# Optimization experiments

Hardware: AMD Instinct MI355X
Metric: run time of the kernel (lower is better)

Reference implementation:

```python
import math
import jax, jax.numpy as jnp
import numpy as np

HEAD_SIZE = 64
DEPTH = 0

def lambda_init_fn(depth):
    depth = depth + 1
    return 0.8 - 0.6 * math.exp(-0.3 * depth)

def setup_inputs() -> dict:
    key = jax.random.key(0)
    ks = jax.random.split(key, 9)
    B, T, C = 4, 4096, 1024
    H2 = 2 * HEAD_SIZE  # 128
    return {
        "x":  jax.random.normal(ks[0], (B, T, C), dtype=jnp.float32),
        "Wq": jax.random.normal(ks[1], (C, H2), dtype=jnp.float32) * (C ** -0.5),
        "Wk": jax.random.normal(ks[2], (C, H2), dtype=jnp.float32) * (C ** -0.5),
        "Wv": jax.random.normal(ks[3], (C, H2), dtype=jnp.float32) * (C ** -0.5),
        "lambda_q1": jax.random.normal(ks[4], (HEAD_SIZE,), dtype=jnp.float32) * 0.1,
        "lambda_q2": jax.random.normal(ks[5], (HEAD_SIZE,), dtype=jnp.float32) * 0.1,
        "lambda_k1": jax.random.normal(ks[6], (HEAD_SIZE,), dtype=jnp.float32) * 0.1,
        "lambda_k2": jax.random.normal(ks[7], (HEAD_SIZE,), dtype=jnp.float32) * 0.1,
    }

def reference(x, Wq, Wk, Wv, lambda_q1, lambda_q2, lambda_k1, lambda_k2):
    B, T, C = x.shape
    q = x @ Wq  # (B,T,2*hs)
    k = x @ Wk
    v = x @ Wv  # (B,T,2*hs)
    q1, q2 = jnp.split(q, 2, axis=-1)
    k1, k2 = jnp.split(k, 2, axis=-1)
    scale = 1.0 / math.sqrt(HEAD_SIZE)
    w1 = jnp.einsum('btd,bsd->bts', q1, k1) * scale  # (B,T,T)
    w2 = jnp.einsum('btd,bsd->bts', q2, k2) * scale
    causal = jnp.tril(jnp.ones((T, T), dtype=bool))
    neg_inf = jnp.float32(-jnp.inf)
    w1 = jnp.where(causal, w1, neg_inf)
    w2 = jnp.where(causal, w2, neg_inf)
    lam1 = jnp.exp(jnp.sum(lambda_q1 * lambda_k1))
    lam2 = jnp.exp(jnp.sum(lambda_q2 * lambda_k2))
    lam = lam1 - lam2 + lambda_init_fn(DEPTH)
    weights = jax.nn.softmax(w1, axis=-1) - lam * jax.nn.softmax(w2, axis=-1)
    out = jnp.einsum('bts,bsd->btd', weights, v)  # (B,T,2*hs)
    return out
```

## Files before the change

kernel.cpp:

```cpp
#include <hip/hip_runtime.h>
#include <hip/hip_bf16.h>

typedef __bf16 bf16x8 __attribute__((ext_vector_type(8)));
typedef float f32x4 __attribute__((ext_vector_type(4)));

#define LAMBDA_INIT 0.3555090675909693f
#define CEXP 0.18033688011112042f

#define K_OFF   ((size_t)16384 * 128)
#define VT_OFF  ((size_t)2 * 16384 * 128)
#define PART_OFF_BYTES ((size_t)12582912)
#define REC_FLOATS 4160

__device__ __forceinline__ unsigned short f2bf(float f) {
    __hip_bfloat16 h = __float2bfloat16(f);
    unsigned short u;
    __builtin_memcpy(&u, &h, 2);
    return u;
}
__device__ __forceinline__ float bf2f(unsigned short u) {
    unsigned int x = ((unsigned int)u) << 16;
    float f;
    __builtin_memcpy(&f, &x, 4);
    return f;
}
__device__ __forceinline__ unsigned int cvt_pk_bf16(float a, float b) {
    unsigned int r;
    asm volatile("v_cvt_pk_bf16_f32 %0, %1, %2" : "=v"(r) : "v"(a), "v"(b));
    return r;
}

__global__ __launch_bounds__(256) void prep_wt(
    const float* __restrict__ Wq, const float* __restrict__ Wk,
    const float* __restrict__ Wv, unsigned short* __restrict__ WT) {
    const int kt = blockIdx.x, nt = blockIdx.y, mat = blockIdx.z;
    const float* W = (mat == 0) ? Wq : (mat == 1) ? Wk : Wv;
    unsigned short* O = WT + (size_t)mat * 128 * 1024;
    __shared__ float tb[64][65];
    const int r = threadIdx.x >> 2, c4 = (threadIdx.x & 3) * 16;
    for (int j = 0; j < 4; ++j) {
        float4 v = *(const float4*)&W[(size_t)(kt * 64 + r) * 128 + nt * 64 + c4 + j * 4];
        tb[r][c4 + j * 4 + 0] = v.x;
        tb[r][c4 + j * 4 + 1] = v.y;
        tb[r][c4 + j * 4 + 2] = v.z;
        tb[r][c4 + j * 4 + 3] = v.w;
    }
    __syncthreads();
    unsigned short tmp[16];
    for (int j = 0; j < 16; ++j) tmp[j] = f2bf(tb[c4 + j][r]);
    *(uint4*)&O[(size_t)(nt * 64 + r) * 1024 + kt * 64 + c4] = *(uint4*)&tmp[0];
    *(uint4*)&O[(size_t)(nt * 64 + r) * 1024 + kt * 64 + c4 + 8] = *(uint4*)&tmp[8];
}

__global__ __launch_bounds__(256, 3) void qkv_gemm(
    const float* __restrict__ x, const unsigned short* __restrict__ WT,
    unsigned short* __restrict__ qkv) {
    const int tid = threadIdx.x;
    const int l = tid & 63, w = tid >> 6;
    const int g = l >> 4, i16 = l & 15;
    const int row0 = blockIdx.x * 64;
    const int mat = blockIdx.y;
    const unsigned short* Wt = WT + (size_t)mat * 128 * 1024;

    __shared__ unsigned short xs[64][72];
    __shared__ unsigned short wt[128][72];

    f32x4 acc[8];
    const f32x4 z4 = {0.f, 0.f, 0.f, 0.f};
    for (int nb = 0; nb < 8; ++nb) acc[nb] = z4;

    const int xr = tid >> 4;
    const int xc = (tid & 15) * 4;
    const int wn = tid >> 3;
    const int wk8 = (tid & 7) * 8;
    const float* xp0 = &x[(size_t)(row0 + xr) * 1024 + xc];
    const unsigned short* wp0 = &Wt[(size_t)wn * 1024 + wk8];

    float4 ax0, ax1, ax2, ax3, bx0, bx1, bx2, bx3;
    uint4 aw0, aw1, aw2, aw3, bw0, bw1, bw2, bw3;

#define QI(k0_, X0, X1, X2, X3, W0, W1, W2, W3) do {                        \
        X0 = *(const float4*)&xp0[(k0_)];                                   \
        X1 = *(const float4*)&xp0[16 * 1024 + (k0_)];                       \
        X2 = *(const float4*)&xp0[32 * 1024 + (k0_)];                       \
        X3 = *(const float4*)&xp0[48 * 1024 + (k0_)];                       \
        W0 = *(const uint4*)&wp0[(k0_)];                                    \
        W1 = *(const uint4*)&wp0[32 * 1024 + (k0_)];                        \
        W2 = *(const uint4*)&wp0[64 * 1024 + (k0_)];                        \
        W3 = *(const uint4*)&wp0[96 * 1024 + (k0_)];                        \
    } while (0)

#define QS(X0, X1, X2, X3, W0, W1, W2, W3) do {                             \
        *(ushort4*)&xs[xr +  0][xc] = make_ushort4(f2bf(X0.x), f2bf(X0.y), f2bf(X0.z), f2bf(X0.w)); \
        *(ushort4*)&xs[xr + 16][xc] = make_ushort4(f2bf(X1.x), f2bf(X1.y), f2bf(X1.z), f2bf(X1.w)); \
        *(ushort4*)&xs[xr + 32][xc] = make_ushort4(f2bf(X2.x), f2bf(X2.y), f2bf(X2.z), f2bf(X2.w)); \
        *(ushort4*)&xs[xr + 48][xc] = make_ushort4(f2bf(X3.x), f2bf(X3.y), f2bf(X3.z), f2bf(X3.w)); \
        *(uint4*)&wt[wn +  0][wk8] = W0;                                    \
        *(uint4*)&wt[wn + 32][wk8] = W1;                                    \
        *(uint4*)&wt[wn + 64][wk8] = W2;                                    \
        *(uint4*)&wt[wn + 96][wk8] = W3;                                    \
    } while (0)

#define QMFMA() do {                                                        \
        bf16x8 af0 = *(const bf16x8*)&xs[w * 16 + i16][8 * g];              \
        bf16x8 af1 = *(const bf16x8*)&xs[w * 16 + i16][32 + 8 * g];         \
        _Pragma("unroll")                                                   \
        for (int nb = 0; nb < 8; ++nb) {                                    \
            bf16x8 b0 = *(const bf16x8*)&wt[nb * 16 + i16][8 * g];          \
            bf16x8 b1 = *(const bf16x8*)&wt[nb * 16 + i16][32 + 8 * g];     \
            acc[nb] = __builtin_amdgcn_mfma_f32_16x16x32_bf16(af0, b0, acc[nb], 0, 0, 0); \
            acc[nb] = __builtin_amdgcn_mfma_f32_16x16x32_bf16(af1, b1, acc[nb], 0, 0, 0); \
        }                                                                   \
    } while (0)

    QI(0, ax0, ax1, ax2, ax3, aw0, aw1, aw2, aw3);
    QI(64, bx0, bx1, bx2, bx3, bw0, bw1, bw2, bw3);
    #pragma unroll 1
    for (int k0 = 0; k0 < 1024; k0 += 128) {
        __syncthreads();
        QS(ax0, ax1, ax2, ax3, aw0, aw1, aw2, aw3);
        if (k0 + 128 < 1024) QI(k0 + 128, ax0, ax1, ax2, ax3, aw0, aw1, aw2, aw3);
        __syncthreads();
        QMFMA();
        __syncthreads();
        QS(bx0, bx1, bx2, bx3, bw0, bw1, bw2, bw3);
        if (k0 + 192 < 1024) QI(k0 + 192, bx0, bx1, bx2, bx3, bw0, bw1, bw2, bw3);
        __syncthreads();
        QMFMA();
    }
#undef QI
#undef QS
#undef QMFMA

    __syncthreads();
    unsigned short(*ts)[136] = (unsigned short(*)[136]) & wt[0][0];
    const float qscale = (mat == 0) ? CEXP : 1.0f;
    for (int nb = 0; nb < 8; ++nb)
        for (int r = 0; r < 4; ++r)
            ts[w * 16 + g * 4 + r][nb * 16 + i16] = f2bf(acc[nb][r] * qscale);
    __syncthreads();

    const int bq = row0 >> 12;
    const int s = (row0 >> 6) & 63;
    if (mat == 0) {
        unsigned short* outp = qkv + (size_t)row0 * 128;
        #pragma unroll
        for (int it = 0; it < 4; ++it) {
            int tr = it * 16 + (tid >> 4), dv0 = (tid & 15) * 8;
            *(uint4*)&outp[tr * 128 + dv0] = *(const uint4*)&ts[tr][dv0];
        }
    } else if (mat == 1) {
        unsigned short* kimg = qkv + K_OFF + ((size_t)(bq * 64 + s) * 2) * 4096;
        #pragma unroll
        for (int it = 0; it < 4; ++it) {
            int lin = it * 256 + tid;
            int branch_ = (lin >> 9) & 1;
            int region = (lin >> 6) & 7;
            int slot = lin & 63;
            int row = (region >> 1) * 16 + (slot & 15);
            int d = branch_ * 64 + (region & 1) * 32 + (slot >> 4) * 8;
            uint4 vv = *(const uint4*)&ts[row][d];
            *(uint4*)&kimg[(size_t)branch_ * 4096 + (region * 64 + slot) * 8] = vv;
        }
    } else {
        unsigned short* vimg = qkv + VT_OFF + (size_t)(bq * 64 + s) * 8192;
        #pragma unroll
        for (int it = 0; it < 4; ++it) {
            int lin = it * 256 + tid;
            int region = lin >> 6;
            int slot = lin & 63;
            int dv = (region >> 1) * 16 + (slot & 15);
            int kv0 = (region & 1) * 32 + (slot >> 4) * 8;
            unsigned short tmp[8];
            #pragma unroll
            for (int e = 0; e < 8; ++e) tmp[e] = ts[kv0 + e][dv];
            *(uint4*)&vimg[(region * 64 + slot) * 8] = *(uint4*)tmp;
        }
    }
}

__global__ __launch_bounds__(256, 3) void diff_attn_pair(
    const unsigned short* __restrict__ q, const unsigned short* __restrict__ kimg,
    const unsigned short* __restrict__ vimg,
    float* __restrict__ part, int ncs) {
    const int bx = blockIdx.x, b = blockIdx.y;
    const int c = blockIdx.z >> 1, branch = blockIdx.z & 1;
    const int bxe = (c & 1) ? (31 - bx) : bx;
    const int t_o = 63 - 2 * bxe, t_e = t_o - 1;
    const int n = t_o + 1;
    const int s_lo = (c * n) >> ncs, smax = ((c + 1) * n) >> ncs;

    if (s_lo >= smax) return;

    const int tid = threadIdx.x;
    const int l = tid & 63, w = tid >> 6;
    const int gq = l >> 4, i16 = l & 15;
    const float NEGINF = -__builtin_inff();

    __shared__ unsigned short ksf[2][4096];
    __shared__ unsigned short psf[8192];

    float* recA = part + ((((size_t)(b * 64 + t_e) << ncs) + c) * 2 + branch) * REC_FLOATS;
    float* recB = part + ((((size_t)(b * 64 + t_o) << ncs) + c) * 2 + branch) * REC_FLOATS;
    const bool emptyA = (s_lo > t_e);

    const size_t bbase = (size_t)b * 4096;
    const unsigned short* kimg_b = kimg + (size_t)b * 524288;
    const unsigned short* vimg_b = vimg + (size_t)b * 524288;
    const int tid8 = tid * 8;
    const int l8 = l * 8;
    const f32x4 z4 = {0.f, 0.f, 0.f, 0.f};

    bf16x8 qfA[2], qfB[2];
    #pragma unroll
    for (int cc = 0; cc < 2; ++cc) {
        qfA[cc] = *(const bf16x8*)&q[(bbase + t_e * 64 + w * 16 + i16) * 128 + branch * 64 + cc * 32 + 8 * gq];
        qfB[cc] = *(const bf16x8*)&q[(bbase + t_o * 64 + w * 16 + i16) * 128 + branch * 64 + cc * 32 + 8 * gq];
    }

    float lsumA = 0.f, lsumB = 0.f;
    f32x4 acc[2][4][2];
    for (int qs = 0; qs < 2; ++qs)
        for (int qg = 0; qg < 4; ++qg)
            for (int j = 0; j < 2; ++j) acc[qs][qg][j] = z4;

    int pdst[4];
    #pragma unroll
    for (int cb = 0; cb < 4; ++cb)
        pdst[cb] = ((w * 2 + (cb >> 1)) * 64 + ((cb & 1) * 2 + (gq >> 1)) * 16 + i16) * 8 + (gq & 1) * 4;

    uint4 kr0, kr1;
    bf16x8 vb00, vb01, vb10, vb11;

#define K_ISSUE(s_) do {                                                            \
        const unsigned short* kp = &kimg_b[((size_t)(s_) * 2 + branch) * 4096];     \
        kr0 = *(const uint4*)&kp[tid8];                                             \
        kr1 = *(const uint4*)&kp[tid8 + 2048];                                      \
    } while (0)
#define V_ISSUE(s_) do {                                                            \
        const unsigned short* vp = &vimg_b[(size_t)(s_) * 8192 + w * 2048];         \
        vb00 = *(const bf16x8*)&vp[l8];                                             \
        vb01 = *(const bf16x8*)&vp[512 + l8];                                       \
        vb10 = *(const bf16x8*)&vp[1024 + l8];                                      \
        vb11 = *(const bf16x8*)&vp[1536 + l8];                                      \
    } while (0)

    K_ISSUE(s_lo);
    V_ISSUE(s_lo);
    int pb = 0;
    #pragma unroll 1
    for (int s = s_lo; s < smax; ++s) {
        *(uint4*)&ksf[pb][tid8] = kr0;
        *(uint4*)&ksf[pb][tid8 + 2048] = kr1;
        if (s + 1 < smax) K_ISSUE(s + 1);
        __syncthreads();
        const bool aAct = (s != t_o);

        f32x4 scA[4], scB[4];
        for (int cb = 0; cb < 4; ++cb) { scA[cb] = z4; scB[cb] = z4; }
        __builtin_amdgcn_s_setprio(1);
        #pragma unroll
        for (int cb = 0; cb < 4; ++cb)
            for (int cc = 0; cc < 2; ++cc) {
                bf16x8 kf = *(const bf16x8*)&ksf[pb][((cb * 2 + cc) * 64 + l) * 8];
                scA[cb] = __builtin_amdgcn_mfma_f32_16x16x32_bf16(kf, qfA[cc], scA[cb], 0, 0, 0);
                scB[cb] = __builtin_amdgcn_mfma_f32_16x16x32_bf16(kf, qfB[cc], scB[cb], 0, 0, 0);
            }
        __builtin_amdgcn_s_setprio(0);

        if (aAct) {
            if (s == t_e) {
                int ql = w * 16 + i16;
                for (int cb = 0; cb < 4; ++cb)
                    for (int r = 0; r < 4; ++r)
                        if (cb * 16 + gq * 4 + r > ql) scA[cb][r] = NEGINF;
            }
            #pragma unroll
            for (int cb = 0; cb < 4; ++cb) {
                float p0 = exp2f(scA[cb][0]);
                float p1 = exp2f(scA[cb][1]);
                float p2 = exp2f(scA[cb][2]);
                float p3 = exp2f(scA[cb][3]);
                lsumA += (p0 + p1) + (p2 + p3);
                uint2 pw;
                pw.x = cvt_pk_bf16(p0, p1);
                pw.y = cvt_pk_bf16(p2, p3);
                *(uint2*)&psf[pdst[cb]] = pw;
            }
        }
        {
            if (s == t_o) {
                int ql = w * 16 + i16;
                for (int cb = 0; cb < 4; ++cb)
                    for (int r = 0; r < 4; ++r)
                        if (cb * 16 + gq * 4 + r > ql) scB[cb][r] = NEGINF;
            }
            #pragma unroll
            for (int cb = 0; cb < 4; ++cb) {
                float p0 = exp2f(scB[cb][0]);
                float p1 = exp2f(scB[cb][1]);
                float p2 = exp2f(scB[cb][2]);
                float p3 = exp2f(scB[cb][3]);
                lsumB += (p0 + p1) + (p2 + p3);
                uint2 pw;
                pw.x = cvt_pk_bf16(p0, p1);
                pw.y = cvt_pk_bf16(p2, p3);
                *(uint2*)&psf[4096 + pdst[cb]] = pw;
            }
        }
        __syncthreads();

        __builtin_amdgcn_s_setprio(1);
        if (aAct) {
            #pragma unroll
            for (int qg = 0; qg < 4; ++qg) {
                bf16x8 pa0 = *(const bf16x8*)&psf[(qg * 2 + 0) * 512 + l8];
                bf16x8 pa1 = *(const bf16x8*)&psf[(qg * 2 + 1) * 512 + l8];
                acc[0][qg][0] = __builtin_amdgcn_mfma_f32_16x16x32_bf16(pa0, vb00, acc[0][qg][0], 0, 0, 0);
                acc[0][qg][0] = __builtin_amdgcn_mfma_f32_16x16x32_bf16(pa1, vb01, acc[0][qg][0], 0, 0, 0);
                acc[0][qg][1] = __builtin_amdgcn_mfma_f32_16x16x32_bf16(pa0, vb10, acc[0][qg][1], 0, 0, 0);
                acc[0][qg][1] = __builtin_amdgcn_mfma_f32_16x16x32_bf16(pa1, vb11, acc[0][qg][1], 0, 0, 0);
            }
        }
        #pragma unroll
        for (int qg = 0; qg < 4; ++qg) {
            bf16x8 pa0 = *(const bf16x8*)&psf[4096 + (qg * 2 + 0) * 512 + l8];
            bf16x8 pa1 = *(const bf16x8*)&psf[4096 + (qg * 2 + 1) * 512 + l8];
            acc[1][qg][0] = __builtin_amdgcn_mfma_f32_16x16x32_bf16(pa0, vb00, acc[1][qg][0], 0, 0, 0);
            acc[1][qg][0] = __builtin_amdgcn_mfma_f32_16x16x32_bf16(pa1, vb01, acc[1][qg][0], 0, 0, 0);
            acc[1][qg][1] = __builtin_amdgcn_mfma_f32_16x16x32_bf16(pa0, vb10, acc[1][qg][1], 0, 0, 0);
            acc[1][qg][1] = __builtin_amdgcn_mfma_f32_16x16x32_bf16(pa1, vb11, acc[1][qg][1], 0, 0, 0);
        }
        __builtin_amdgcn_s_setprio(0);
        if (s + 1 < smax) V_ISSUE(s + 1);
        pb ^= 1;
    }
#undef K_ISSUE
#undef V_ISSUE

    lsumA += __shfl_xor(lsumA, 16);
    lsumA += __shfl_xor(lsumA, 32);
    lsumB += __shfl_xor(lsumB, 16);
    lsumB += __shfl_xor(lsumB, 32);
    if (!emptyA) {
        if (gq == 0) recA[w * 16 + i16] = lsumA;
        unsigned short* OA = (unsigned short*)(recA + 64);
        for (int qg = 0; qg < 4; ++qg)
            for (int j = 0; j < 2; ++j)
                for (int r = 0; r < 4; ++r)
                    OA[(qg * 16 + gq * 4 + r) * 128 + (w * 2 + j) * 16 + i16] = f2bf(acc[0][qg][j][r]);
    }
    {
        if (gq == 0) recB[w * 16 + i16] = lsumB;
        unsigned short* OB = (unsigned short*)(recB + 64);
        for (int qg = 0; qg < 4; ++qg)
            for (int j = 0; j < 2; ++j)
                for (int r = 0; r < 4; ++r)
                    OB[(qg * 16 + gq * 4 + r) * 128 + (w * 2 + j) * 16 + i16] = f2bf(acc[1][qg][j][r]);
    }
}

__global__ __launch_bounds__(256) void diff_combine(
    const float* __restrict__ part,
    const float* __restrict__ lq1, const float* __restrict__ lq2,
    const float* __restrict__ lk1, const float* __restrict__ lk2,
    float* __restrict__ out, int ncs) {
    const int t = blockIdx.x, b = blockIdx.y;
    const int tid = threadIdx.x;
    const int nc = 1 << ncs;
    const int n = (t | 1) + 1;
    __shared__ float sl[2][64];
    __shared__ float s_lam;

    const float* recbase = part + (((size_t)(b * 64 + t) << ncs)) * 2 * REC_FLOATS;

    if (tid < 64) {
        float s1 = lq1[tid] * lk1[tid];
        float s2 = lq2[tid] * lk2[tid];
        for (int off = 32; off > 0; off >>= 1) {
            s1 += __shfl_xor(s1, off);
            s2 += __shfl_xor(s2, off);
        }
        if (tid == 0) s_lam = expf(s1) - expf(s2) + LAMBDA_INIT;
    }
    if (tid < 128) {
        int r = tid & 63, br = tid >> 6;
        float acc = 0.f;
        for (int c = 0; c < nc; ++c) {
            int lo = (c * n) >> ncs, hi = ((c + 1) * n) >> ncs;
            if (lo >= hi || lo > t) continue;
            acc += recbase[(c * 2 + br) * REC_FLOATS + r];
        }
        sl[br][r] = acc;
    }
    __syncthreads();
    const float lam = s_lam;

    float* op = out + ((size_t)b * 4096 + (size_t)t * 64) * 128;
    for (int grp = 0; grp < 4; ++grp) {
        int gid = grp * 256 + tid;
        int e = gid * 8;
        int row = e >> 7;
        float o1[8] = {0, 0, 0, 0, 0, 0, 0, 0}, o2[8] = {0, 0, 0, 0, 0, 0, 0, 0};
        for (int c = 0; c < nc; ++c) {
            int lo = (c * n) >> ncs, hi = ((c + 1) * n) >> ncs;
            if (lo >= hi || lo > t) continue;
            const unsigned short* O0 = (const unsigned short*)(recbase + (c * 2 + 0) * REC_FLOATS + 64);
            const unsigned short* O1 = (const unsigned short*)(recbase + (c * 2 + 1) * REC_FLOATS + 64);
            uint4 u0 = *(const uint4*)&O0[e];
            uint4 u1 = *(const uint4*)&O1[e];
            const unsigned short* e0 = (const unsigned short*)&u0;
            const unsigned short* e1 = (const unsigned short*)&u1;
            #pragma unroll
            for (int j = 0; j < 8; ++j) {
                o1[j] += bf2f(e0[j]);
                o2[j] += bf2f(e1[j]);
            }
        }
        float l1inv = 1.0f / sl[0][row], l2inv = 1.0f / sl[1][row];
        float res[8];
        #pragma unroll
        for (int j = 0; j < 8; ++j) res[j] = o1[j] * l1inv - lam * o2[j] * l2inv;
        *(float4*)&op[e] = *(float4*)&res[0];
        *(float4*)&op[e + 4] = *(float4*)&res[4];
    }
}

extern "C" void kernel_launch(void* const* d_in, const int* in_sizes, int n_in,
                              void* d_out, int out_size, void* d_ws, size_t ws_size,
                              hipStream_t stream) {
    const float* x   = (const float*)d_in[0];
    const float* Wq  = (const float*)d_in[1];
    const float* Wk  = (const float*)d_in[2];
    const float* Wv  = (const float*)d_in[3];
    const float* lq1 = (const float*)d_in[4];
    const float* lq2 = (const float*)d_in[5];
    const float* lk1 = (const float*)d_in[6];
    const float* lk2 = (const float*)d_in[7];
    float* out = (float*)d_out;
    unsigned short* qkv = (unsigned short*)d_ws;

    const int ncs = 2;
    const size_t part_bytes = (size_t)256 * (1 << ncs) * 2 * REC_FLOATS * 4;
    float* part = (float*)((char*)d_ws + PART_OFF_BYTES);
    unsigned short* WT = (unsigned short*)((char*)d_ws + PART_OFF_BYTES + part_bytes);

    prep_wt<<<dim3(16, 2, 3), 256, 0, stream>>>(Wq, Wk, Wv, WT);
    qkv_gemm<<<dim3(256, 3), 256, 0, stream>>>(x, WT, qkv);

    const unsigned short* qb = qkv;
    const unsigned short* kb = qkv + K_OFF;
    const unsigned short* vtb = qkv + VT_OFF;
    diff_attn_pair<<<dim3(32, 4, 2 << ncs), 256, 0, stream>>>(qb, kb, vtb, part, ncs);
    diff_combine<<<dim3(64, 4), 256, 0, stream>>>(part, lq1, lq2, lk1, lk2, out, ncs);
}
```

Baseline: 97.82 us.

## Fuse Q, K, V projections into one GEMM block per row tile

Replaces the three-way grid over Q/K/V matrices with a single 512-thread block per 64-row tile that computes all 384 output columns at once. Each x tile is then loaded and converted to bf16 only once instead of three times, which cuts global reads of the fp32 input. In exchange, each block needs more shared memory for a 384-row weight tile and has fewer blocks in flight (256 instead of 768), which may lower occupancy and latency hiding.

```diff
diff --git a/kernel.cpp b/kernel.cpp
--- a/kernel.cpp
+++ b/kernel.cpp
@@ -52,79 +52,82 @@
     *(uint4*)&O[(size_t)(nt * 64 + r) * 1024 + kt * 64 + c4 + 8] = *(uint4*)&tmp[8];
 }
 
-__global__ __launch_bounds__(256, 3) void qkv_gemm(
+__global__ __launch_bounds__(512) void qkv_fused(
     const float* __restrict__ x, const unsigned short* __restrict__ WT,
     unsigned short* __restrict__ qkv) {
     const int tid = threadIdx.x;
     const int l = tid & 63, w = tid >> 6;
     const int g = l >> 4, i16 = l & 15;
+    const int rh = w >> 2, cp = w & 3;
     const int row0 = blockIdx.x * 64;
-    const int mat = blockIdx.y;
-    const unsigned short* Wt = WT + (size_t)mat * 128 * 1024;
 
     __shared__ unsigned short xs[64][72];
-    __shared__ unsigned short wt[128][72];
-
-    f32x4 acc[8];
+    __shared__ unsigned short wt[384][72];
+
+    f32x4 acc[2][6];
     const f32x4 z4 = {0.f, 0.f, 0.f, 0.f};
-    for (int nb = 0; nb < 8; ++nb) acc[nb] = z4;
-
-    const int xr = tid >> 4;
-    const int xc = (tid & 15) * 4;
-    const int wn = tid >> 3;
-    const int wk8 = (tid & 7) * 8;
-    const float* xp0 = &x[(size_t)(row0 + xr) * 1024 + xc];
-    const unsigned short* wp0 = &Wt[(size_t)wn * 1024 + wk8];
-
-    float4 ax0, ax1, ax2, ax3, bx0, bx1, bx2, bx3;
-    uint4 aw0, aw1, aw2, aw3, bw0, bw1, bw2, bw3;
-
-#define QI(k0_, X0, X1, X2, X3, W0, W1, W2, W3) do {                        \
-        X0 = *(const float4*)&xp0[(k0_)];                                   \
-        X1 = *(const float4*)&xp0[16 * 1024 + (k0_)];                       \
-        X2 = *(const float4*)&xp0[32 * 1024 + (k0_)];                       \
-        X3 = *(const float4*)&xp0[48 * 1024 + (k0_)];                       \
-        W0 = *(const uint4*)&wp0[(k0_)];                                    \
-        W1 = *(const uint4*)&wp0[32 * 1024 + (k0_)];                        \
-        W2 = *(const uint4*)&wp0[64 * 1024 + (k0_)];                        \
-        W3 = *(const uint4*)&wp0[96 * 1024 + (k0_)];                        \
+    for (int rt = 0; rt < 2; ++rt)
+        for (int ct = 0; ct < 6; ++ct) acc[rt][ct] = z4;
+
+    const int xrow = tid >> 3, xcol = (tid & 7) * 8;
+    const int wn = tid >> 3, wk8 = (tid & 7) * 8;
+    const float* xp = &x[(size_t)(row0 + xrow) * 1024 + xcol];
+    const unsigned short* wp = &WT[(size_t)wn * 1024 + wk8];
+
+    float4 ax0, ax1, bx0, bx1;
+    uint4 aw0, aw1, aw2, aw3, aw4, aw5, bw0, bw1, bw2, bw3, bw4, bw5;
+
+#define QI(k0_, X0, X1, W0, W1, W2, W3, W4, W5) do {                        \
+        X0 = *(const float4*)&xp[(k0_)];                                    \
+        X1 = *(const float4*)&xp[(k0_) + 4];                                \
+        W0 = *(const uint4*)&wp[(k0_)];                                     \
+        W1 = *(const uint4*)&wp[64 * 1024 + (k0_)];                         \
+        W2 = *(const uint4*)&wp[128 * 1024 + (k0_)];                        \
+        W3 = *(const uint4*)&wp[192 * 1024 + (k0_)];                        \
+        W4 = *(const uint4*)&wp[256 * 1024 + (k0_)];                        \
+        W5 = *(const uint4*)&wp[320 * 1024 + (k0_)];                        \
     } while (0)
 
-#define QS(X0, X1, X2, X3, W0, W1, W2, W3) do {                             \
-        *(ushort4*)&xs[xr +  0][xc] = make_ushort4(f2bf(X0.x), f2bf(X0.y), f2bf(X0.z), f2bf(X0.w)); \
-        *(ushort4*)&xs[xr + 16][xc] = make_ushort4(f2bf(X1.x), f2bf(X1.y), f2bf(X1.z), f2bf(X1.w)); \
-        *(ushort4*)&xs[xr + 32][xc] = make_ushort4(f2bf(X2.x), f2bf(X2.y), f2bf(X2.z), f2bf(X2.w)); \
-        *(ushort4*)&xs[xr + 48][xc] = make_ushort4(f2bf(X3.x), f2bf(X3.y), f2bf(X3.z), f2bf(X3.w)); \
-        *(uint4*)&wt[wn +  0][wk8] = W0;                                    \
-        *(uint4*)&wt[wn + 32][wk8] = W1;                                    \
-        *(uint4*)&wt[wn + 64][wk8] = W2;                                    \
-        *(uint4*)&wt[wn + 96][wk8] = W3;                                    \
+#define QS(X0, X1, W0, W1, W2, W3, W4, W5) do {                             \
+        *(ushort4*)&xs[xrow][xcol]     = make_ushort4(f2bf(X0.x), f2bf(X0.y), f2bf(X0.z), f2bf(X0.w)); \
+        *(ushort4*)&xs[xrow][xcol + 4] = make_ushort4(f2bf(X1.x), f2bf(X1.y), f2bf(X1.z), f2bf(X1.w)); \
+        *(uint4*)&wt[wn +   0][wk8] = W0;                                   \
+        *(uint4*)&wt[wn +  64][wk8] = W1;                                   \
+        *(uint4*)&wt[wn + 128][wk8] = W2;                                   \
+        *(uint4*)&wt[wn + 192][wk8] = W3;                                   \
+        *(uint4*)&wt[wn + 256][wk8] = W4;                                   \
+        *(uint4*)&wt[wn + 320][wk8] = W5;                                   \
     } while (0)
 
 #define QMFMA() do {                                                        \
-        bf16x8 af0 = *(const bf16x8*)&xs[w * 16 + i16][8 * g];              \
-        bf16x8 af1 = *(const bf16x8*)&xs[w * 16 + i16][32 + 8 * g];         \
+        bf16x8 af[2][2];                                                    \
         _Pragma("unroll")                                                   \
-        for (int nb = 0; nb < 8; ++nb) {                                    \
-            bf16x8 b0 = *(const bf16x8*)&wt[nb * 16 + i16][8 * g];          \
-            bf16x8 b1 = *(const bf16x8*)&wt[nb * 16 + i16][32 + 8 * g];     \
-            acc[nb] = __builtin_amdgcn_mfma_f32_16x16x32_bf16(af0, b0, acc[nb], 0, 0, 0); \
-            acc[nb] = __builtin_amdgcn_mfma_f32_16x16x32_bf16(af1, b1, acc[nb], 0, 0, 0); \
+        for (int rt = 0; rt < 2; ++rt)                                      \
+            for (int cc = 0; cc < 2; ++cc)                                  \
+                af[rt][cc] = *(const bf16x8*)&xs[rh * 32 + rt * 16 + i16][cc * 32 + 8 * g]; \
+        _Pragma("unroll")                                                   \
+        for (int ct = 0; ct < 6; ++ct) {                                    \
+            _Pragma("unroll")                                               \
+            for (int cc = 0; cc < 2; ++cc) {                                \
+                bf16x8 bb = *(const bf16x8*)&wt[cp * 96 + ct * 16 + i16][cc * 32 + 8 * g]; \
+                for (int rt = 0; rt < 2; ++rt)                              \
+                    acc[rt][ct] = __builtin_amdgcn_mfma_f32_16x16x32_bf16(af[rt][cc], bb, acc[rt][ct], 0, 0, 0); \
+            }                                                               \
         }                                                                   \
     } while (0)
 
-    QI(0, ax0, ax1, ax2, ax3, aw0, aw1, aw2, aw3);
-    QI(64, bx0, bx1, bx2, bx3, bw0, bw1, bw2, bw3);
+    QI(0, ax0, ax1, aw0, aw1, aw2, aw3, aw4, aw5);
+    QI(64, bx0, bx1, bw0, bw1, bw2, bw3, bw4, bw5);
     #pragma unroll 1
     for (int k0 = 0; k0 < 1024; k0 += 128) {
         __syncthreads();
-        QS(ax0, ax1, ax2, ax3, aw0, aw1, aw2, aw3);
-        if (k0 + 128 < 1024) QI(k0 + 128, ax0, ax1, ax2, ax3, aw0, aw1, aw2, aw3);
+        QS(ax0, ax1, aw0, aw1, aw2, aw3, aw4, aw5);
+        if (k0 + 128 < 1024) QI(k0 + 128, ax0, ax1, aw0, aw1, aw2, aw3, aw4, aw5);
         __syncthreads();
         QMFMA();
         __syncthreads();
-        QS(bx0, bx1, bx2, bx3, bw0, bw1, bw2, bw3);
-        if (k0 + 192 < 1024) QI(k0 + 192, bx0, bx1, bx2, bx3, bw0, bw1, bw2, bw3);
+        QS(bx0, bx1, bw0, bw1, bw2, bw3, bw4, bw5);
+        if (k0 + 192 < 1024) QI(k0 + 192, bx0, bx1, bw0, bw1, bw2, bw3, bw4, bw5);
         __syncthreads();
         QMFMA();
     }
@@ -133,43 +136,48 @@
 #undef QMFMA
 
     __syncthreads();
-    unsigned short(*ts)[136] = (unsigned short(*)[136]) & wt[0][0];
-    const float qscale = (mat == 0) ? CEXP : 1.0f;
-    for (int nb = 0; nb < 8; ++nb)
-        for (int r = 0; r < 4; ++r)
-            ts[w * 16 + g * 4 + r][nb * 16 + i16] = f2bf(acc[nb][r] * qscale);
+    unsigned short(*ts)[392] = (unsigned short(*)[392]) & wt[0][0];
+    #pragma unroll
+    for (int rt = 0; rt < 2; ++rt)
+        for (int ct = 0; ct < 6; ++ct) {
+            const float sc = (cp * 96 + ct * 16 < 128) ? CEXP : 1.0f;
+            for (int r = 0; r < 4; ++r)
+                ts[rh * 32 + rt * 16 + g * 4 + r][cp * 96 + ct * 16 + i16] = f2bf(acc[rt][ct][r] * sc);
+        }
     __syncthreads();
 
     const int bq = row0 >> 12;
     const int s = (row0 >> 6) & 63;
-    if (mat == 0) {
+    {
         unsigned short* outp = qkv + (size_t)row0 * 128;
         #pragma unroll
-        for (int it = 0; it < 4; ++it) {
-            int tr = it * 16 + (tid >> 4), dv0 = (tid & 15) * 8;
+        for (int it = 0; it < 2; ++it) {
+            int tr = it * 32 + (tid >> 4), dv0 = (tid & 15) * 8;
             *(uint4*)&outp[tr * 128 + dv0] = *(const uint4*)&ts[tr][dv0];
         }
-    } else if (mat == 1) {
+    }
+    {
         unsigned short* kimg = qkv + K_OFF + ((size_t)(bq * 64 + s) * 2) * 4096;
         #pragma unroll
-        for (int it = 0; it < 4; ++it) {
-            int lin = it * 256 + tid;
+        for (int it = 0; it < 2; ++it) {
+            int lin = it * 512 + tid;
             int branch_ = (lin >> 9) & 1;
             int region = (lin >> 6) & 7;
             int slot = lin & 63;
             int row = (region >> 1) * 16 + (slot & 15);
-            int d = branch_ * 64 + (region & 1) * 32 + (slot >> 4) * 8;
+            int d = 128 + branch_ * 64 + (region & 1) * 32 + (slot >> 4) * 8;
             uint4 vv = *(const uint4*)&ts[row][d];
             *(uint4*)&kimg[(size_t)branch_ * 4096 + (region * 64 + slot) * 8] = vv;
         }
-    } else {
+    }
+    {
         unsigned short* vimg = qkv + VT_OFF + (size_t)(bq * 64 + s) * 8192;
         #pragma unroll
-        for (int it = 0; it < 4; ++it) {
-            int lin = it * 256 + tid;
-            int region = lin >> 6;
+        for (int it = 0; it < 2; ++it) {
+            int lin = it * 512 + tid;
+            int region = (lin >> 6) & 15;
             int slot = lin & 63;
-            int dv = (region >> 1) * 16 + (slot & 15);
+            int dv = 256 + (region >> 1) * 16 + (slot & 15);
             int kv0 = (region & 1) * 32 + (slot >> 4) * 8;
             unsigned short tmp[8];
             #pragma unroll
@@ -446,7 +454,7 @@
     unsigned short* WT = (unsigned short*)((char*)d_ws + PART_OFF_BYTES + part_bytes);
 
     prep_wt<<<dim3(16, 2, 3), 256, 0, stream>>>(Wq, Wk, Wv, WT);
-    qkv_gemm<<<dim3(256, 3), 256, 0, stream>>>(x, WT, qkv);
+    qkv_fused<<<256, 512, 0, stream>>>(x, WT, qkv);
 
     const unsigned short* qb = qkv;
     const unsigned short* kb = qkv + K_OFF;
```

Result: faster. 92.89 us (-5.0%).
